# Kernel optimization log

Hardware: AMD Instinct MI355X
Metric: run time of the kernel (lower is better)

## Reference

```python
import jax, jax.numpy as jnp
import numpy as np

N = 100000        # total nodes (60000 type-0 + 40000 type-1)
E = 1600000       # edges (avg degree 16)
D = 128           # num_hidden
C = 16            # num_classes


def _glorot(key, fan_in, fan_out):
    # xavier_normal with gain 1.414 (as in the torch module inits)
    std = 1.414 * (2.0 / (fan_in + fan_out)) ** 0.5
    return jax.random.normal(key, (fan_in, fan_out), jnp.float32) * std


def setup_inputs() -> dict:
    key = jax.random.key(0)
    ks = jax.random.split(key, 12)
    feat0 = jax.random.normal(ks[0], (60000, 512), jnp.float32)
    feat1 = jax.random.normal(ks[1], (40000, 256), jnp.float32)
    src = jax.random.randint(ks[2], (E,), 0, N, jnp.int32)
    dst = jax.random.randint(ks[3], (E,), 0, N, jnp.int32)
    return {
        "feat0": feat0,
        "feat1": feat1,
        "src": src,
        "dst": dst,
        "W_fc0": _glorot(ks[4], 512, D), "b_fc0": jnp.zeros((D,), jnp.float32),
        "W_fc1": _glorot(ks[5], 256, D), "b_fc1": jnp.zeros((D,), jnp.float32),
        "W_g0": _glorot(ks[6], D, D),   "b_g0": jnp.zeros((D,), jnp.float32),
        "W_g1": _glorot(ks[7], D, D),   "b_g1": jnp.zeros((D,), jnp.float32),
        "W_out": _glorot(ks[8], D, C),  "b_out": jnp.zeros((C,), jnp.float32),
    }


def reference(feat0, feat1, src, dst,
              W_fc0, b_fc0, W_fc1, b_fc1,
              W_g0, b_g0, W_g1, b_g1, W_out, b_out):
    # per-type input projections, then concat over node types -> (N, D)
    h = jnp.concatenate([feat0 @ W_fc0 + b_fc0, feat1 @ W_fc1 + b_fc1], axis=0)

    # in-degree for 'mean' reduce (DGL mean yields 0 for isolated nodes; clamp avoids /0)
    deg = jax.ops.segment_sum(jnp.ones((E,), jnp.float32), dst, num_segments=N)
    inv_deg = (1.0 / jnp.maximum(deg, 1.0))[:, None]

    def gin(h, W, b):
        # copy_u + mean reduce: neigh[i] = mean_{(j->i) in E} h[j]
        neigh = jax.ops.segment_sum(h[src], dst, num_segments=N) * inv_deg
        # (1 + eps) * h + neigh with eps = 0, then apply_func (Linear), then sigmoid
        return jax.nn.sigmoid((h + neigh) @ W + b)

    h = gin(h, W_g0, b_g0)      # gat_layers[0]
    h = gin(h, W_g1, b_g1)      # gat_layers[1]
    logits = gin(h, W_out, b_out)  # gat_layers[-1] -> (N, C)
    # logits.unsqueeze(1).mean(1) is a no-op
    return logits
```

## Files before the change

kernel.cpp:

```cpp
#include <hip/hip_runtime.h>
#include <hip/hip_bf16.h>

#define N_NODES 100000
#define N0_ROWS 60000
#define N1_ROWS 40000
#define NE 1600000
#define HD 128
#define NB 782
#define BSH 128
#define EPB 2560
#define NBLK 625

typedef __attribute__((ext_vector_type(8))) short short8;
typedef __attribute__((ext_vector_type(4))) float f32x4;
typedef __attribute__((ext_vector_type(2))) float f32x2;

__device__ __forceinline__ float bf16lo(unsigned v) { return __uint_as_float(v << 16); }
__device__ __forceinline__ float bf16hi(unsigned v) { return __uint_as_float(v & 0xFFFF0000u); }

__device__ __forceinline__ unsigned short f2bf_rne(float f) {
    unsigned u = __float_as_uint(f);
    return (unsigned short)((u + 0x7FFFu + ((u >> 16) & 1u)) >> 16);
}
__device__ __forceinline__ unsigned pack2_rne(float lo, float hi) {
    unsigned a = __float_as_uint(lo); a = (a + 0x7FFFu + ((a >> 16) & 1u)) >> 16;
    unsigned b = __float_as_uint(hi); b = (b + 0x7FFFu + ((b >> 16) & 1u)) & 0xFFFF0000u;
    return (a & 0xFFFFu) | b;
}
__device__ __forceinline__ float sigmoidf_(float v) { return 1.0f / (1.0f + __expf(-v)); }

#if defined(__has_builtin)
#if __has_builtin(__builtin_amdgcn_cvt_pk_fp8_f32) && __has_builtin(__builtin_amdgcn_cvt_pk_f32_fp8)
#define HAS_FP8_CVT 1
#endif
#endif

#ifdef HAS_FP8_CVT
__device__ __forceinline__ unsigned pack4_fp8(float c0, float c1, float c2, float c3) {
    int r = 0;
    r = __builtin_amdgcn_cvt_pk_fp8_f32(c0, c1, r, false);
    r = __builtin_amdgcn_cvt_pk_fp8_f32(c2, c3, r, true);
    return (unsigned)r;
}
__device__ __forceinline__ f32x2 unpack2_fp8(unsigned u16) {
    return __builtin_amdgcn_cvt_pk_f32_fp8((int)u16, false);
}
#else
__device__ __forceinline__ unsigned enc1_fp8(float f) {
    f = fminf(448.f, fmaxf(-448.f, f));
    float a = fabsf(f);
    unsigned s = (__float_as_uint(f) >> 31) << 7;
    if (a >= 0.015625f) {
        unsigned u = __float_as_uint(a);
        u += 0x7FFFFu + ((u >> 20) & 1u);
        int E = (int)((u >> 23) & 255) - 120;
        unsigned m3 = (u >> 20) & 7;
        if (E > 15) { E = 15; m3 = 6; }
        return s | ((unsigned)E << 3) | m3;
    } else {
        int q = (int)rintf(a * 512.f);
        if (q >= 8) return s | (1u << 3);
        return s | (unsigned)q;
    }
}
__device__ __forceinline__ unsigned pack4_fp8(float c0, float c1, float c2, float c3) {
    return enc1_fp8(c0) | (enc1_fp8(c1) << 8) | (enc1_fp8(c2) << 16) | (enc1_fp8(c3) << 24);
}
__device__ __forceinline__ float dec1_fp8(unsigned b) {
    unsigned s = (b >> 7) & 1, e = (b >> 3) & 15, m = b & 7;
    float v = e ? ldexpf((float)(8 + m), (int)e - 10) : ldexpf((float)m, -9);
    return s ? -v : v;
}
__device__ __forceinline__ f32x2 unpack2_fp8(unsigned u16) {
    f32x2 r;
    r[0] = dec1_fp8(u16 & 0xFFu);
    r[1] = dec1_fp8((u16 >> 8) & 0xFFu);
    return r;
}
#endif

__global__ __launch_bounds__(256) void k_phist(const int* __restrict__ dst,
                                               int* __restrict__ cnt) {
    __shared__ int h[NB];
    int blk = blockIdx.x;
    for (int i = threadIdx.x; i < NB; i += 256) h[i] = 0;
    __syncthreads();
    int e0 = blk * EPB;
    for (int e = e0 + threadIdx.x; e < e0 + EPB; e += 256)
        atomicAdd(&h[dst[e] >> 7], 1);
    __syncthreads();
    for (int i = threadIdx.x; i < NB; i += 256)
        cnt[i * NBLK + blk] = h[i];
}

__global__ __launch_bounds__(64) void k_colscan(int* __restrict__ cnt,
                                                int* __restrict__ bcnt) {
    int b = blockIdx.x, lane = threadIdx.x & 63;
    int* col = cnt + (size_t)b * NBLK;
    int carry = 0;
    for (int base = 0; base < NBLK; base += 64) {
        int i = base + lane;
        int v = (i < NBLK) ? col[i] : 0;
        int s = v;
        #pragma unroll
        for (int off = 1; off < 64; off <<= 1) {
            int t = __shfl_up(s, off);
            if (lane >= off) s += t;
        }
        if (i < NBLK) col[i] = carry + s - v;
        carry += __shfl(s, 63);
    }
    if (lane == 0) bcnt[b] = carry;
}

__global__ void k_bscan(const int* __restrict__ bcnt, int* __restrict__ boff,
                        int* __restrict__ rowptr) {
    int lane = threadIdx.x & 63;
    const int CH = (NB + 63) / 64;
    int base = lane * CH;
    int t = 0;
    for (int c = 0; c < CH; ++c) {
        int i = base + c;
        t += (i < NB) ? bcnt[i] : 0;
    }
    int s = t;
    #pragma unroll
    for (int off = 1; off < 64; off <<= 1) {
        int u = __shfl_up(s, off);
        if (lane >= off) s += u;
    }
    int running = s - t;
    for (int c = 0; c < CH; ++c) {
        int i = base + c;
        if (i < NB) {
            boff[i] = running;
            running += bcnt[i];
        }
    }
    if (lane == 0) { boff[NB] = NE; rowptr[N_NODES] = NE; }
}

__global__ __launch_bounds__(256) void k_pplace(const int* __restrict__ src,
                                                const int* __restrict__ dst,
                                                const int* __restrict__ boff,
                                                const int* __restrict__ cnt,
                                                unsigned* __restrict__ ebuf) {
    __shared__ int h[NB];
    int blk = blockIdx.x;
    for (int i = threadIdx.x; i < NB; i += 256) h[i] = cnt[i * NBLK + blk];
    __syncthreads();
    int e0 = blk * EPB;
    for (int e = e0 + threadIdx.x; e < e0 + EPB; e += 256) {
        int d = dst[e];
        int b = d >> 7;
        int pos = atomicAdd(&h[b], 1);
        ebuf[boff[b] + pos] = ((unsigned)(d & 127) << 17) | (unsigned)src[e];
    }
}

__global__ __launch_bounds__(256) void k_bplace(const unsigned* __restrict__ ebuf,
                                                const int* __restrict__ boff,
                                                int* __restrict__ rowptr,
                                                float* __restrict__ invd,
                                                int* __restrict__ eidx) {
    __shared__ int cnt[BSH], off[BSH], lcnt[BSH];
    int b = blockIdx.x, tid = threadIdx.x;
    int e0 = boff[b], e1 = boff[b + 1];
    for (int i = tid; i < BSH; i += 256) { cnt[i] = 0; lcnt[i] = 0; }
    __syncthreads();
    for (int e = e0 + tid; e < e1; e += 256)
        atomicAdd(&cnt[ebuf[e] >> 17], 1);
    __syncthreads();
    if (tid < 64) {
        int lane = tid;
        int c0 = cnt[2 * lane], c1 = cnt[2 * lane + 1];
        int t = c0 + c1, s = t;
        #pragma unroll
        for (int o = 1; o < 64; o <<= 1) {
            int u = __shfl_up(s, o);
            if (lane >= o) s += u;
        }
        int excl = s - t;
        off[2 * lane] = excl;
        off[2 * lane + 1] = excl + c0;
    }
    __syncthreads();
    for (int i = tid; i < BSH; i += 256) {
        int node = b * BSH + i;
        if (node < N_NODES) {
            rowptr[node] = e0 + off[i];
            invd[node] = 1.0f / fmaxf((float)cnt[i], 1.0f);
        }
    }
    for (int e = e0 + tid; e < e1; e += 256) {
        unsigned ent = ebuf[e];
        int d = ent >> 17;
        int pos = e0 + off[d] + atomicAdd(&lcnt[d], 1);
        eidx[pos] = (int)(ent & 0x1FFFFu);
    }
}

__global__ void prep_w_all(const float* __restrict__ W0, unsigned short* __restrict__ T0,
                           const float* __restrict__ W1, unsigned short* __restrict__ T1,
                           const float* __restrict__ W2, unsigned short* __restrict__ T2,
                           const float* __restrict__ W3, unsigned short* __restrict__ T3,
                           const float* __restrict__ W4, unsigned short* __restrict__ T4) {
    int gid = blockIdx.x * blockDim.x + threadIdx.x;
    int stride = gridDim.x * blockDim.x;
    const int S0 = 512 * 128, S1 = 256 * 128, S2 = 128 * 128, S3 = 128 * 128, S4 = 128 * 16;
    const int E1 = S0 + S1, E2 = E1 + S2, E3 = E2 + S3, E4 = E3 + S4;
    for (int i = gid; i < E4; i += stride) {
        if (i < S0) {
            int n = i / 512, k = i - n * 512;
            T0[i] = f2bf_rne(W0[k * 128 + n]);
        } else if (i < E1) {
            int j = i - S0; int n = j / 256, k = j - n * 256;
            T1[j] = f2bf_rne(W1[k * 128 + n]);
        } else if (i < E2) {
            int j = i - E1; int n = j / 128, k = j - n * 128;
            T2[j] = f2bf_rne(W2[k * 128 + n]);
        } else if (i < E3) {
            int j = i - E2; int n = j / 128, k = j - n * 128;
            T3[j] = f2bf_rne(W3[k * 128 + n]);
        } else {
            int j = i - E3; int n = j / 128, k = j - n * 128;
            T4[j] = f2bf_rne(W4[k * 16 + n]);
        }
    }
}

template <int K>
__global__ __launch_bounds__(512, 4) void k_proj_fused(const float* __restrict__ feat,
                                                       const unsigned short* __restrict__ Wt,
                                                       const float* __restrict__ bias,
                                                       const unsigned short* __restrict__ Wg,
                                                       unsigned short* __restrict__ zout,
                                                       unsigned* __restrict__ z8out,
                                                       int ntiles, int row_off) {
    constexpr int KC = K / 32;
    __shared__ unsigned short A_lds[16][K + 8];
    __shared__ unsigned short h_lds[16][HD + 8];

    const int tid = threadIdx.x;
    const int lane = tid & 63, w = tid >> 6;
    const int g = lane >> 4, r16 = lane & 15;
    const int col = w * 16 + r16;

    short8 fb[KC];
    #pragma unroll
    for (int kc = 0; kc < KC; ++kc)
        fb[kc] = *reinterpret_cast<const short8*>(Wt + (size_t)col * K + kc * 32 + g * 8);
    short8 fbg[4];
    #pragma unroll
    for (int kc = 0; kc < 4; ++kc)
        fbg[kc] = *reinterpret_cast<const short8*>(Wg + (size_t)col * HD + kc * 32 + g * 8);
    const float bv = bias[col];

    const int srow = tid >> 5;
    const int sseg = tid & 31;

    for (int tile = blockIdx.x; tile < ntiles; tile += gridDim.x) {
        __syncthreads();
        const float4* rowp = reinterpret_cast<const float4*>(feat + (size_t)(tile * 16 + srow) * K);
        #pragma unroll
        for (int s = 0; s < K / 128; ++s) {
            float4 v = rowp[sseg + s * 32];
            unsigned lo = __builtin_amdgcn_perm(__float_as_uint(v.y), __float_as_uint(v.x), 0x07060302u);
            unsigned hi = __builtin_amdgcn_perm(__float_as_uint(v.w), __float_as_uint(v.z), 0x07060302u);
            *reinterpret_cast<uint2*>(&A_lds[srow][(sseg + s * 32) * 4]) = make_uint2(lo, hi);
        }
        __syncthreads();
        f32x4 acc = {0.f, 0.f, 0.f, 0.f};
        #pragma unroll
        for (int kc = 0; kc < KC; ++kc) {
            short8 fa = *reinterpret_cast<const short8*>(&A_lds[r16][kc * 32 + g * 8]);
            acc = __builtin_amdgcn_mfma_f32_16x16x32_bf16(fa, fb[kc], acc, 0, 0, 0);
        }
        #pragma unroll
        for (int r = 0; r < 4; ++r)
            h_lds[g * 4 + r][col] = f2bf_rne(acc[r] + bv);
        __syncthreads();
        f32x4 accz = {0.f, 0.f, 0.f, 0.f};
        #pragma unroll
        for (int kc = 0; kc < 4; ++kc) {
            short8 fa = *reinterpret_cast<const short8*>(&h_lds[r16][kc * 32 + g * 8]);
            accz = __builtin_amdgcn_mfma_f32_16x16x32_bf16(fa, fbg[kc], accz, 0, 0, 0);
        }
        #pragma unroll
        for (int r = 0; r < 4; ++r) {
            size_t orow = (size_t)(row_off + tile * 16 + g * 4 + r);
            zout[orow * HD + col] = f2bf_rne(accz[r]);
        }
        __syncthreads();
        #pragma unroll
        for (int r = 0; r < 4; ++r)
            h_lds[g * 4 + r][col] = f2bf_rne(accz[r]);
        __syncthreads();
        {
            int c4 = sseg * 4;
            unsigned p = pack4_fp8(
                bf16lo((unsigned)h_lds[srow][c4])     ,
                bf16lo((unsigned)h_lds[srow][c4 + 1]) ,
                bf16lo((unsigned)h_lds[srow][c4 + 2]) ,
                bf16lo((unsigned)h_lds[srow][c4 + 3]) );
            z8out[(size_t)(row_off + tile * 16 + srow) * 32 + sseg] = p;
        }
    }
}

__global__ __launch_bounds__(256, 4) void k_z_gemm(const unsigned short* __restrict__ x,
                                                   const unsigned short* __restrict__ Wt,
                                                   unsigned short* __restrict__ zout,
                                                   unsigned* __restrict__ z8out) {
    __shared__ unsigned short h_lds[16][HD + 8];
    const int lane = threadIdx.x & 63, wid = threadIdx.x >> 6;
    const int g = lane >> 4, r16 = lane & 15;
    const int colbase = wid * 32;
    const int prow = threadIdx.x >> 4;
    const int pseg = threadIdx.x & 15;

    short8 fb[2][4];
    #pragma unroll
    for (int nt = 0; nt < 2; ++nt) {
        int n = colbase + nt * 16 + r16;
        #pragma unroll
        for (int kc = 0; kc < 4; ++kc)
            fb[nt][kc] = *reinterpret_cast<const short8*>(Wt + (size_t)n * HD + kc * 32 + g * 8);
    }

    const int ntiles = N_NODES / 16;
    for (int tile = blockIdx.x; tile < ntiles; tile += gridDim.x) {
        const unsigned short* ap = x + (size_t)(tile * 16 + r16) * HD;
        f32x4 acc0 = {0.f, 0.f, 0.f, 0.f};
        f32x4 acc1 = {0.f, 0.f, 0.f, 0.f};
        #pragma unroll
        for (int kc = 0; kc < 4; ++kc) {
            short8 fa = *reinterpret_cast<const short8*>(ap + kc * 32 + g * 8);
            acc0 = __builtin_amdgcn_mfma_f32_16x16x32_bf16(fa, fb[0][kc], acc0, 0, 0, 0);
            acc1 = __builtin_amdgcn_mfma_f32_16x16x32_bf16(fa, fb[1][kc], acc1, 0, 0, 0);
        }
        __syncthreads();
        #pragma unroll
        for (int r = 0; r < 4; ++r) {
            size_t orow = (size_t)(tile * 16 + g * 4 + r);
            unsigned short zb0 = f2bf_rne(acc0[r]);
            unsigned short zb1 = f2bf_rne(acc1[r]);
            zout[orow * HD + colbase + r16]      = zb0;
            zout[orow * HD + colbase + 16 + r16] = zb1;
            h_lds[g * 4 + r][colbase + r16]      = zb0;
            h_lds[g * 4 + r][colbase + 16 + r16] = zb1;
        }
        __syncthreads();
        {
            int c8 = pseg * 8;
            unsigned p0 = pack4_fp8(
                bf16lo((unsigned)h_lds[prow][c8])     ,
                bf16lo((unsigned)h_lds[prow][c8 + 1]) ,
                bf16lo((unsigned)h_lds[prow][c8 + 2]) ,
                bf16lo((unsigned)h_lds[prow][c8 + 3]) );
            unsigned p1 = pack4_fp8(
                bf16lo((unsigned)h_lds[prow][c8 + 4]) ,
                bf16lo((unsigned)h_lds[prow][c8 + 5]) ,
                bf16lo((unsigned)h_lds[prow][c8 + 6]) ,
                bf16lo((unsigned)h_lds[prow][c8 + 7]) );
            *reinterpret_cast<uint2*>(&z8out[(size_t)(tile * 16 + prow) * 32 + pseg * 2]) =
                make_uint2(p0, p1);
        }
    }
}

__global__ __launch_bounds__(256, 4) void k_aggz8(const unsigned short* __restrict__ z,
                                                  const unsigned short* __restrict__ z8,
                                                  const int* __restrict__ rowptr,
                                                  const int* __restrict__ eidx,
                                                  const float* __restrict__ invd,
                                                  const float* __restrict__ bias,
                                                  unsigned short* __restrict__ hout) {
    const unsigned* zp = reinterpret_cast<const unsigned*>(z);
    unsigned* hp = reinterpret_cast<unsigned*>(hout);
    int lane = threadIdx.x & 63, wid = threadIdx.x >> 6;
    float blo = bias[2 * lane], bhi = bias[2 * lane + 1];
    int nwaves = gridDim.x * 4;
    for (int node = blockIdx.x * 4 + wid; node < N_NODES; node += nwaves) {
        int rp0 = rowptr[node], rp1 = rowptr[node + 1];
        float a0 = 0.f, a1 = 0.f, b0 = 0.f, b1 = 0.f;
        for (int base = rp0; base < rp1; base += 64) {
            int m = rp1 - base; if (m > 64) m = 64;
            int idx = (lane < m) ? eidx[base + lane] : 0;
            int t = 0;
            for (; t + 4 <= m; t += 4) {
                int j0 = __shfl(idx, t), j1 = __shfl(idx, t + 1);
                int j2 = __shfl(idx, t + 2), j3 = __shfl(idx, t + 3);
                unsigned u0 = z8[(size_t)j0 * 64 + lane];
                unsigned u1 = z8[(size_t)j1 * 64 + lane];
                unsigned u2 = z8[(size_t)j2 * 64 + lane];
                unsigned u3 = z8[(size_t)j3 * 64 + lane];
                f32x2 d0 = unpack2_fp8(u0), d1 = unpack2_fp8(u1);
                f32x2 d2 = unpack2_fp8(u2), d3 = unpack2_fp8(u3);
                a0 += d0[0] + d1[0]; a1 += d0[1] + d1[1];
                b0 += d2[0] + d3[0]; b1 += d2[1] + d3[1];
            }
            for (; t < m; ++t) {
                int j = __shfl(idx, t);
                f32x2 d = unpack2_fp8(z8[(size_t)j * 64 + lane]);
                a0 += d[0]; a1 += d[1];
            }
        }
        a0 += b0; a1 += b1;
        unsigned zv = zp[(size_t)node * 64 + lane];
        float s = invd[node];
        hp[(size_t)node * 64 + lane] = pack2_rne(sigmoidf_(bf16lo(zv) + s * a0 + blo),
                                                 sigmoidf_(bf16hi(zv) + s * a1 + bhi));
    }
}

__global__ __launch_bounds__(256, 4) void k_zout_gemm(const unsigned short* __restrict__ x,
                                                      const unsigned short* __restrict__ Wt,
                                                      unsigned short* __restrict__ z3) {
    const int lane = threadIdx.x & 63, wid = threadIdx.x >> 6;
    const int g = lane >> 4, r16 = lane & 15;

    short8 fb[4];
    #pragma unroll
    for (int kc = 0; kc < 4; ++kc)
        fb[kc] = *reinterpret_cast<const short8*>(Wt + (size_t)r16 * HD + kc * 32 + g * 8);

    const int ntiles = N_NODES / 16;
    for (int tile = blockIdx.x * 4 + wid; tile < ntiles; tile += gridDim.x * 4) {
        const unsigned short* ap = x + (size_t)(tile * 16 + r16) * HD;
        f32x4 acc = {0.f, 0.f, 0.f, 0.f};
        #pragma unroll
        for (int kc = 0; kc < 4; ++kc) {
            short8 fa = *reinterpret_cast<const short8*>(ap + kc * 32 + g * 8);
            acc = __builtin_amdgcn_mfma_f32_16x16x32_bf16(fa, fb[kc], acc, 0, 0, 0);
        }
        #pragma unroll
        for (int r = 0; r < 4; ++r)
            z3[(size_t)(tile * 16 + g * 4 + r) * 16 + r16] = f2bf_rne(acc[r]);
    }
}

__global__ __launch_bounds__(256, 4) void k_agg16(const unsigned short* __restrict__ z3,
                                                  const int* __restrict__ rowptr,
                                                  const int* __restrict__ eidx,
                                                  const float* __restrict__ invd,
                                                  const float* __restrict__ bias,
                                                  float* __restrict__ out) {
    const unsigned* zp = reinterpret_cast<const unsigned*>(z3);
    int lane = threadIdx.x & 63, wid = threadIdx.x >> 6;
    int grp = lane >> 3, sub = lane & 7;
    float blo = bias[2 * sub], bhi = bias[2 * sub + 1];
    int step = gridDim.x * 32;
    for (int nb = blockIdx.x * 32 + wid * 8; nb < N_NODES; nb += step) {
        int node = nb + grp;
        bool valid = node < N_NODES;
        int rp0 = valid ? rowptr[node] : 0;
        int rp1 = valid ? rowptr[node + 1] : 0;
        float a0 = 0.f, a1 = 0.f;
        for (int base = rp0; base < rp1; base += 8) {
            int m = rp1 - base; if (m > 8) m = 8;
            int idx = (sub < m) ? eidx[base + sub] : 0;
            #pragma unroll
            for (int t = 0; t < 8; ++t) {
                if (t < m) {
                    int j = __shfl(idx, (grp << 3) + t);
                    unsigned v = zp[(size_t)j * 8 + sub];
                    a0 += bf16lo(v); a1 += bf16hi(v);
                }
            }
        }
        if (valid) {
            unsigned zv = zp[(size_t)node * 8 + sub];
            float s = invd[node];
            out[(size_t)node * 16 + sub * 2]     = sigmoidf_(bf16lo(zv) + s * a0 + blo);
            out[(size_t)node * 16 + sub * 2 + 1] = sigmoidf_(bf16hi(zv) + s * a1 + bhi);
        }
    }
}

extern "C" void kernel_launch(void* const* d_in, const int* in_sizes, int n_in,
                              void* d_out, int out_size, void* d_ws, size_t ws_size,
                              hipStream_t stream) {
    const float* feat0 = (const float*)d_in[0];
    const float* feat1 = (const float*)d_in[1];
    const int*   src   = (const int*)d_in[2];
    const int*   dst   = (const int*)d_in[3];
    const float* Wfc0  = (const float*)d_in[4];
    const float* bfc0  = (const float*)d_in[5];
    const float* Wfc1  = (const float*)d_in[6];
    const float* bfc1  = (const float*)d_in[7];
    const float* Wg0   = (const float*)d_in[8];
    const float* bg0   = (const float*)d_in[9];
    const float* Wg1   = (const float*)d_in[10];
    const float* bg1   = (const float*)d_in[11];
    const float* Wout  = (const float*)d_in[12];
    const float* bout  = (const float*)d_in[13];

    char* w = (char*)d_ws;
    auto alloc = [&](size_t bytes) {
        char* p = w;
        w += (bytes + 255) & ~(size_t)255;
        return p;
    };
    unsigned short* zA  = (unsigned short*)alloc((size_t)N_NODES * HD * 2);
    unsigned short* zB  = (unsigned short*)alloc((size_t)N_NODES * HD * 2);
    unsigned short* h   = (unsigned short*)alloc((size_t)N_NODES * HD * 2);
    unsigned* z8A = (unsigned*)alloc((size_t)N_NODES * HD);
    unsigned* z8B = (unsigned*)alloc((size_t)N_NODES * HD);
    unsigned short* z3  = (unsigned short*)alloc((size_t)N_NODES * 16 * 2);
    int*   rowptr = (int*)alloc((size_t)(N_NODES + 1) * 4);
    float* invd   = (float*)alloc((size_t)N_NODES * 4);
    int*   eidx   = (int*)alloc((size_t)NE * 4);
    unsigned* ebuf = (unsigned*)alloc((size_t)NE * 4);
    int*   cnt    = (int*)alloc((size_t)NB * NBLK * 4);
    int*   bcnt   = (int*)alloc((size_t)NB * 4);
    int*   boff   = (int*)alloc((size_t)(NB + 1) * 4);
    unsigned short* Wt_fc0 = (unsigned short*)alloc(512 * 128 * 2);
    unsigned short* Wt_fc1 = (unsigned short*)alloc(256 * 128 * 2);
    unsigned short* Wt_g0  = (unsigned short*)alloc(128 * 128 * 2);
    unsigned short* Wt_g1  = (unsigned short*)alloc(128 * 128 * 2);
    unsigned short* Wt_out = (unsigned short*)alloc(128 * 16 * 2);

    k_phist<<<NBLK, 256, 0, stream>>>(dst, cnt);
    k_colscan<<<NB, 64, 0, stream>>>(cnt, bcnt);
    k_bscan<<<1, 64, 0, stream>>>(bcnt, boff, rowptr);
    k_pplace<<<NBLK, 256, 0, stream>>>(src, dst, boff, cnt, ebuf);
    k_bplace<<<NB, 256, 0, stream>>>(ebuf, boff, rowptr, invd, eidx);

    prep_w_all<<<520, 256, 0, stream>>>(Wfc0, Wt_fc0, Wfc1, Wt_fc1,
                                        Wg0, Wt_g0, Wg1, Wt_g1, Wout, Wt_out);

    k_proj_fused<512><<<512, 512, 0, stream>>>(feat0, Wt_fc0, bfc0, Wt_g0, zA, z8A, N0_ROWS / 16, 0);
    k_proj_fused<256><<<512, 512, 0, stream>>>(feat1, Wt_fc1, bfc1, Wt_g0, zA, z8A, N1_ROWS / 16, N0_ROWS);

    k_aggz8<<<2048, 256, 0, stream>>>(zA, (const unsigned short*)z8A, rowptr, eidx, invd, bg0, h);
    k_z_gemm<<<2084, 256, 0, stream>>>(h, Wt_g1, zB, z8B);
    k_aggz8<<<2048, 256, 0, stream>>>(zB, (const unsigned short*)z8B, rowptr, eidx, invd, bg1, h);
    k_zout_gemm<<<1563, 256, 0, stream>>>(h, Wt_out, z3);
    k_agg16<<<2048, 256, 0, stream>>>(z3, rowptr, eidx, invd, bout, (float*)d_out);
}
```

Before: 277.1 us.

## Process two nodes per wave in aggregation, prefetch proj tiles, fuse weight prep

The fp8 neighbour aggregation now gives each half-wave its own node, with lanes reading 4 fp8 values (one 32-bit word) per neighbour row. This halves the lanes per 128-byte row and doubles the node-level parallelism per wave. The projection kernel prefetches the next tile's features into registers while the current tile computes. Weight transposition is merged into the histogram kernel, which also uses fewer, larger edge blocks, saving a launch. The cost is more register pressure and more serial edge loops per half-wave on high-degree nodes.

```diff
diff --git a/kernel.cpp b/kernel.cpp
--- a/kernel.cpp
+++ b/kernel.cpp
@@ -8,8 +8,8 @@
 #define HD 128
 #define NB 782
 #define BSH 128
-#define EPB 2560
-#define NBLK 625
+#define EPB 6400
+#define NBLK 250
 
 typedef __attribute__((ext_vector_type(8))) short short8;
 typedef __attribute__((ext_vector_type(4))) float f32x4;
@@ -42,8 +42,9 @@
     r = __builtin_amdgcn_cvt_pk_fp8_f32(c2, c3, r, true);
     return (unsigned)r;
 }
-__device__ __forceinline__ f32x2 unpack2_fp8(unsigned u16) {
-    return __builtin_amdgcn_cvt_pk_f32_fp8((int)u16, false);
+template <bool HI>
+__device__ __forceinline__ f32x2 unpack2_fp8(unsigned u) {
+    return __builtin_amdgcn_cvt_pk_f32_fp8((int)u, HI);
 }
 #else
 __device__ __forceinline__ unsigned enc1_fp8(float f) {
@@ -71,26 +72,58 @@
     float v = e ? ldexpf((float)(8 + m), (int)e - 10) : ldexpf((float)m, -9);
     return s ? -v : v;
 }
-__device__ __forceinline__ f32x2 unpack2_fp8(unsigned u16) {
+template <bool HI>
+__device__ __forceinline__ f32x2 unpack2_fp8(unsigned u) {
+    unsigned x = HI ? (u >> 16) : u;
     f32x2 r;
-    r[0] = dec1_fp8(u16 & 0xFFu);
-    r[1] = dec1_fp8((u16 >> 8) & 0xFFu);
+    r[0] = dec1_fp8(x & 0xFFu);
+    r[1] = dec1_fp8((x >> 8) & 0xFFu);
     return r;
 }
 #endif
 
-__global__ __launch_bounds__(256) void k_phist(const int* __restrict__ dst,
-                                               int* __restrict__ cnt) {
-    __shared__ int h[NB];
+__global__ __launch_bounds__(256) void k_phist_prep(const int* __restrict__ dst,
+                                                    int* __restrict__ cnt,
+                                                    const float* __restrict__ W0, unsigned short* __restrict__ T0,
+                                                    const float* __restrict__ W1, unsigned short* __restrict__ T1,
+                                                    const float* __restrict__ W2, unsigned short* __restrict__ T2,
+                                                    const float* __restrict__ W3, unsigned short* __restrict__ T3,
+                                                    const float* __restrict__ W4, unsigned short* __restrict__ T4) {
     int blk = blockIdx.x;
-    for (int i = threadIdx.x; i < NB; i += 256) h[i] = 0;
-    __syncthreads();
-    int e0 = blk * EPB;
-    for (int e = e0 + threadIdx.x; e < e0 + EPB; e += 256)
-        atomicAdd(&h[dst[e] >> 7], 1);
-    __syncthreads();
-    for (int i = threadIdx.x; i < NB; i += 256)
-        cnt[i * NBLK + blk] = h[i];
+    if (blk < NBLK) {
+        __shared__ int h[NB];
+        for (int i = threadIdx.x; i < NB; i += 256) h[i] = 0;
+        __syncthreads();
+        int e0 = blk * EPB;
+        for (int e = e0 + threadIdx.x; e < e0 + EPB; e += 256)
+            atomicAdd(&h[dst[e] >> 7], 1);
+        __syncthreads();
+        for (int i = threadIdx.x; i < NB; i += 256)
+            cnt[i * NBLK + blk] = h[i];
+    } else {
+        int gid = (blk - NBLK) * 256 + threadIdx.x;
+        int stride = (gridDim.x - NBLK) * 256;
+        const int S0 = 512 * 128, S1 = 256 * 128, S2 = 128 * 128, S3 = 128 * 128, S4 = 128 * 16;
+        const int E1 = S0 + S1, E2 = E1 + S2, E3 = E2 + S3, E4 = E3 + S4;
+        for (int i = gid; i < E4; i += stride) {
+            if (i < S0) {
+                int n = i / 512, k = i - n * 512;
+                T0[i] = f2bf_rne(W0[k * 128 + n]);
+            } else if (i < E1) {
+                int j = i - S0; int n = j / 256, k = j - n * 256;
+                T1[j] = f2bf_rne(W1[k * 128 + n]);
+            } else if (i < E2) {
+                int j = i - E1; int n = j / 128, k = j - n * 128;
+                T2[j] = f2bf_rne(W2[k * 128 + n]);
+            } else if (i < E3) {
+                int j = i - E2; int n = j / 128, k = j - n * 128;
+                T3[j] = f2bf_rne(W3[k * 128 + n]);
+            } else {
+                int j = i - E3; int n = j / 128, k = j - n * 128;
+                T4[j] = f2bf_rne(W4[k * 16 + n]);
+            }
+        }
+    }
 }
 
 __global__ __launch_bounds__(64) void k_colscan(int* __restrict__ cnt,
@@ -200,35 +233,6 @@
     }
 }
 
-__global__ void prep_w_all(const float* __restrict__ W0, unsigned short* __restrict__ T0,
-                           const float* __restrict__ W1, unsigned short* __restrict__ T1,
-                           const float* __restrict__ W2, unsigned short* __restrict__ T2,
-                           const float* __restrict__ W3, unsigned short* __restrict__ T3,
-                           const float* __restrict__ W4, unsigned short* __restrict__ T4) {
-    int gid = blockIdx.x * blockDim.x + threadIdx.x;
-    int stride = gridDim.x * blockDim.x;
-    const int S0 = 512 * 128, S1 = 256 * 128, S2 = 128 * 128, S3 = 128 * 128, S4 = 128 * 16;
-    const int E1 = S0 + S1, E2 = E1 + S2, E3 = E2 + S3, E4 = E3 + S4;
-    for (int i = gid; i < E4; i += stride) {
-        if (i < S0) {
-            int n = i / 512, k = i - n * 512;
-            T0[i] = f2bf_rne(W0[k * 128 + n]);
-        } else if (i < E1) {
-            int j = i - S0; int n = j / 256, k = j - n * 256;
-            T1[j] = f2bf_rne(W1[k * 128 + n]);
-        } else if (i < E2) {
-            int j = i - E1; int n = j / 128, k = j - n * 128;
-            T2[j] = f2bf_rne(W2[k * 128 + n]);
-        } else if (i < E3) {
-            int j = i - E2; int n = j / 128, k = j - n * 128;
-            T3[j] = f2bf_rne(W3[k * 128 + n]);
-        } else {
-            int j = i - E3; int n = j / 128, k = j - n * 128;
-            T4[j] = f2bf_rne(W4[k * 16 + n]);
-        }
-    }
-}
-
 template <int K>
 __global__ __launch_bounds__(512, 4) void k_proj_fused(const float* __restrict__ feat,
                                                        const unsigned short* __restrict__ Wt,
@@ -238,6 +242,7 @@
                                                        unsigned* __restrict__ z8out,
                                                        int ntiles, int row_off) {
     constexpr int KC = K / 32;
+    constexpr int NSEG = K / 128;
     __shared__ unsigned short A_lds[16][K + 8];
     __shared__ unsigned short h_lds[16][HD + 8];
 
@@ -259,17 +264,29 @@
     const int srow = tid >> 5;
     const int sseg = tid & 31;
 
-    for (int tile = blockIdx.x; tile < ntiles; tile += gridDim.x) {
-        __syncthreads();
+    float4 pre[NSEG];
+    int tile = blockIdx.x;
+    if (tile < ntiles) {
         const float4* rowp = reinterpret_cast<const float4*>(feat + (size_t)(tile * 16 + srow) * K);
         #pragma unroll
-        for (int s = 0; s < K / 128; ++s) {
-            float4 v = rowp[sseg + s * 32];
-            unsigned lo = __builtin_amdgcn_perm(__float_as_uint(v.y), __float_as_uint(v.x), 0x07060302u);
-            unsigned hi = __builtin_amdgcn_perm(__float_as_uint(v.w), __float_as_uint(v.z), 0x07060302u);
+        for (int s = 0; s < NSEG; ++s) pre[s] = rowp[sseg + s * 32];
+    }
+
+    for (; tile < ntiles; tile += gridDim.x) {
+        __syncthreads();
+        #pragma unroll
+        for (int s = 0; s < NSEG; ++s) {
+            unsigned lo = __builtin_amdgcn_perm(__float_as_uint(pre[s].y), __float_as_uint(pre[s].x), 0x07060302u);
+            unsigned hi = __builtin_amdgcn_perm(__float_as_uint(pre[s].w), __float_as_uint(pre[s].z), 0x07060302u);
             *reinterpret_cast<uint2*>(&A_lds[srow][(sseg + s * 32) * 4]) = make_uint2(lo, hi);
         }
         __syncthreads();
+        int nt = tile + gridDim.x;
+        if (nt < ntiles) {
+            const float4* rowp = reinterpret_cast<const float4*>(feat + (size_t)(nt * 16 + srow) * K);
+            #pragma unroll
+            for (int s = 0; s < NSEG; ++s) pre[s] = rowp[sseg + s * 32];
+        }
         f32x4 acc = {0.f, 0.f, 0.f, 0.f};
         #pragma unroll
         for (int kc = 0; kc < KC; ++kc) {
@@ -370,47 +387,61 @@
 }
 
 __global__ __launch_bounds__(256, 4) void k_aggz8(const unsigned short* __restrict__ z,
-                                                  const unsigned short* __restrict__ z8,
+                                                  const unsigned* __restrict__ z8,
                                                   const int* __restrict__ rowptr,
                                                   const int* __restrict__ eidx,
                                                   const float* __restrict__ invd,
                                                   const float* __restrict__ bias,
                                                   unsigned short* __restrict__ hout) {
-    const unsigned* zp = reinterpret_cast<const unsigned*>(z);
-    unsigned* hp = reinterpret_cast<unsigned*>(hout);
-    int lane = threadIdx.x & 63, wid = threadIdx.x >> 6;
-    float blo = bias[2 * lane], bhi = bias[2 * lane + 1];
+    const uint2* zp2 = reinterpret_cast<const uint2*>(z);
+    uint2* hp2 = reinterpret_cast<uint2*>(hout);
+    const int lane = threadIdx.x & 63, wid = threadIdx.x >> 6;
+    const int half = lane >> 5, l32 = lane & 31;
+    const float4 bvec = *reinterpret_cast<const float4*>(&bias[4 * l32]);
+    const int npairs = N_NODES / 2;
     int nwaves = gridDim.x * 4;
-    for (int node = blockIdx.x * 4 + wid; node < N_NODES; node += nwaves) {
+    for (int pair = blockIdx.x * 4 + wid; pair < npairs; pair += nwaves) {
+        int node = pair * 2 + half;
         int rp0 = rowptr[node], rp1 = rowptr[node + 1];
-        float a0 = 0.f, a1 = 0.f, b0 = 0.f, b1 = 0.f;
-        for (int base = rp0; base < rp1; base += 64) {
-            int m = rp1 - base; if (m > 64) m = 64;
-            int idx = (lane < m) ? eidx[base + lane] : 0;
+        float a0 = 0.f, a1 = 0.f, a2 = 0.f, a3 = 0.f;
+        for (int base = rp0; base < rp1; base += 32) {
+            int m = rp1 - base; if (m > 32) m = 32;
+            int idx = (l32 < m) ? eidx[base + l32] : 0;
             int t = 0;
             for (; t + 4 <= m; t += 4) {
-                int j0 = __shfl(idx, t), j1 = __shfl(idx, t + 1);
-                int j2 = __shfl(idx, t + 2), j3 = __shfl(idx, t + 3);
-                unsigned u0 = z8[(size_t)j0 * 64 + lane];
-                unsigned u1 = z8[(size_t)j1 * 64 + lane];
-                unsigned u2 = z8[(size_t)j2 * 64 + lane];
-                unsigned u3 = z8[(size_t)j3 * 64 + lane];
-                f32x2 d0 = unpack2_fp8(u0), d1 = unpack2_fp8(u1);
-                f32x2 d2 = unpack2_fp8(u2), d3 = unpack2_fp8(u3);
-                a0 += d0[0] + d1[0]; a1 += d0[1] + d1[1];
-                b0 += d2[0] + d3[0]; b1 += d2[1] + d3[1];
+                int j0 = __shfl(idx, half * 32 + t);
+                int j1 = __shfl(idx, half * 32 + t + 1);
+                int j2 = __shfl(idx, half * 32 + t + 2);
+                int j3 = __shfl(idx, half * 32 + t + 3);
+                unsigned u0 = z8[(size_t)j0 * 32 + l32];
+                unsigned u1 = z8[(size_t)j1 * 32 + l32];
+                unsigned u2 = z8[(size_t)j2 * 32 + l32];
+                unsigned u3 = z8[(size_t)j3 * 32 + l32];
+                f32x2 p;
+                p = unpack2_fp8<false>(u0); a0 += p[0]; a1 += p[1];
+                p = unpack2_fp8<true >(u0); a2 += p[0]; a3 += p[1];
+                p = unpack2_fp8<false>(u1); a0 += p[0]; a1 += p[1];
+                p = unpack2_fp8<true >(u1); a2 += p[0]; a3 += p[1];
+                p = unpack2_fp8<false>(u2); a0 += p[0]; a1 += p[1];
+                p = unpack2_fp8<true >(u2); a2 += p[0]; a3 += p[1];
+                p = unpack2_fp8<false>(u3); a0 += p[0]; a1 += p[1];
+                p = unpack2_fp8<true >(u3); a2 += p[0]; a3 += p[1];
             }
             for (; t < m; ++t) {
-                int j = __shfl(idx, t);
-                f32x2 d = unpack2_fp8(z8[(size_t)j * 64 + lane]);
-                a0 += d[0]; a1 += d[1];
+                int j = __shfl(idx, half * 32 + t);
+                unsigned u = z8[(size_t)j * 32 + l32];
+                f32x2 p;
+                p = unpack2_fp8<false>(u); a0 += p[0]; a1 += p[1];
+                p = unpack2_fp8<true >(u); a2 += p[0]; a3 += p[1];
             }
         }
-        a0 += b0; a1 += b1;
-        unsigned zv = zp[(size_t)node * 64 + lane];
+        uint2 sv = zp2[(size_t)node * 32 + l32];
         float s = invd[node];
-        hp[(size_t)node * 64 + lane] = pack2_rne(sigmoidf_(bf16lo(zv) + s * a0 + blo),
-                                                 sigmoidf_(bf16hi(zv) + s * a1 + bhi));
+        float o0 = sigmoidf_(bf16lo(sv.x) + s * a0 + bvec.x);
+        float o1 = sigmoidf_(bf16hi(sv.x) + s * a1 + bvec.y);
+        float o2 = sigmoidf_(bf16lo(sv.y) + s * a2 + bvec.z);
+        float o3 = sigmoidf_(bf16hi(sv.y) + s * a3 + bvec.w);
+        hp2[(size_t)node * 32 + l32] = make_uint2(pack2_rne(o0, o1), pack2_rne(o2, o3));
     }
 }
 
@@ -521,21 +552,20 @@
     unsigned short* Wt_g1  = (unsigned short*)alloc(128 * 128 * 2);
     unsigned short* Wt_out = (unsigned short*)alloc(128 * 16 * 2);
 
-    k_phist<<<NBLK, 256, 0, stream>>>(dst, cnt);
+    k_phist_prep<<<NBLK + 70, 256, 0, stream>>>(dst, cnt,
+                                                Wfc0, Wt_fc0, Wfc1, Wt_fc1,
+                                                Wg0, Wt_g0, Wg1, Wt_g1, Wout, Wt_out);
     k_colscan<<<NB, 64, 0, stream>>>(cnt, bcnt);
     k_bscan<<<1, 64, 0, stream>>>(bcnt, boff, rowptr);
     k_pplace<<<NBLK, 256, 0, stream>>>(src, dst, boff, cnt, ebuf);
     k_bplace<<<NB, 256, 0, stream>>>(ebuf, boff, rowptr, invd, eidx);
 
-    prep_w_all<<<520, 256, 0, stream>>>(Wfc0, Wt_fc0, Wfc1, Wt_fc1,
-                                        Wg0, Wt_g0, Wg1, Wt_g1, Wout, Wt_out);
-
     k_proj_fused<512><<<512, 512, 0, stream>>>(feat0, Wt_fc0, bfc0, Wt_g0, zA, z8A, N0_ROWS / 16, 0);
     k_proj_fused<256><<<512, 512, 0, stream>>>(feat1, Wt_fc1, bfc1, Wt_g0, zA, z8A, N1_ROWS / 16, N0_ROWS);
 
-    k_aggz8<<<2048, 256, 0, stream>>>(zA, (const unsigned short*)z8A, rowptr, eidx, invd, bg0, h);
+    k_aggz8<<<2048, 256, 0, stream>>>(zA, z8A, rowptr, eidx, invd, bg0, h);
     k_z_gemm<<<2084, 256, 0, stream>>>(h, Wt_g1, zB, z8B);
-    k_aggz8<<<2048, 256, 0, stream>>>(zB, (const unsigned short*)z8B, rowptr, eidx, invd, bg1, h);
+    k_aggz8<<<2048, 256, 0, stream>>>(zB, z8B, rowptr, eidx, invd, bg1, h);
     k_zout_gemm<<<1563, 256, 0, stream>>>(h, Wt_out, z3);
     k_agg16<<<2048, 256, 0, stream>>>(z3, rowptr, eidx, invd, bout, (float*)d_out);
 }
```

Result: faster. 250.5 us, median of 2 (-9.6%).
